# Performance work log

Measured on AMD Instinct MI355X. Metric: run time of the kernel, lower is better.

The kernel has to match this reference:

```python
import jax, jax.numpy as jnp
import numpy as np

N = 8192
IN_C = 512
OUT_C = 512


def setup_inputs() -> dict:
    key = jax.random.key(0)
    k1, k2, k3 = jax.random.split(key, 3)
    x = jax.random.normal(k1, (N, IN_C), dtype=jnp.float32)
    adj = jax.random.uniform(k2, (N, N), dtype=jnp.float32)
    # torch.rand initializer for the weight (uniform [0,1))
    w = jax.random.uniform(k3, (IN_C, OUT_C), dtype=jnp.float32)
    return {"x": x, "adj": adj, "w": w}


def reference(x, adj, w):
    # A = adj + I
    A = adj + jnp.eye(adj.shape[0], dtype=adj.dtype)
    # D_hat = diag(deg)^{-1/2}; diagonal inverse + sqrt == elementwise rsqrt of degrees
    deg = jnp.sum(A, axis=1)                      # [N]
    d_inv_sqrt = jax.lax.rsqrt(deg)               # [N]
    # A_hat = D_hat @ A @ D_hat == row/col scaling (same math, no dense inverse)
    A_hat = A * d_inv_sqrt[:, None] * d_inv_sqrt[None, :]
    mm_1 = A_hat @ x                              # [N, in_c]
    return jax.nn.elu(mm_1 @ w)                   # [N, out_c]
```

## Files before the change

### kernel.cpp

```cpp
#include <hip/hip_runtime.h>

#define NN 8192
#define CC 512

typedef __attribute__((ext_vector_type(8))) short short8;
typedef __attribute__((ext_vector_type(4))) float f32x4;
typedef unsigned short ushort_t;

__device__ __forceinline__ unsigned short f2bf(float f) {
    unsigned int u = __float_as_uint(f);
    u += 0x7FFF + ((u >> 16) & 1);
    return (unsigned short)(u >> 16);
}

__device__ __forceinline__ void gload_lds16(const void* g, void* l) {
    __builtin_amdgcn_global_load_lds((const __attribute__((address_space(1))) unsigned int*)g,
                                     (__attribute__((address_space(3))) unsigned int*)l,
                                     16, 0, 0);
}

__global__ __launch_bounds__(256) void k_rowsum_cvt(const float* __restrict__ adj,
                                                    float* __restrict__ ds,
                                                    ushort_t* __restrict__ adj16) {
    int row = blockIdx.x;
    const float4* p = (const float4*)(adj + (size_t)row * NN);
    ushort4* q = (ushort4*)(adj16 + (size_t)row * NN);
    float s = 0.f;
#pragma unroll
    for (int i = 0; i < 8; ++i) {
        float4 v = p[threadIdx.x + i * 256];
        s += (v.x + v.y) + (v.z + v.w);
        ushort4 u;
        u.x = f2bf(v.x); u.y = f2bf(v.y); u.z = f2bf(v.z); u.w = f2bf(v.w);
        q[threadIdx.x + i * 256] = u;
    }
#pragma unroll
    for (int off = 32; off > 0; off >>= 1) s += __shfl_down(s, off, 64);
    __shared__ float partial[4];
    if ((threadIdx.x & 63) == 0) partial[threadIdx.x >> 6] = s;
    __syncthreads();
    if (threadIdx.x == 0) {
        float deg = ((partial[0] + partial[1]) + (partial[2] + partial[3])) + 1.0f;
        ds[row] = rsqrtf(deg);
    }
}

__global__ __launch_bounds__(256) void k_rowsum(const float* __restrict__ adj,
                                                float* __restrict__ ds) {
    int row = blockIdx.x;
    const float4* p = (const float4*)(adj + (size_t)row * NN);
    float s = 0.f;
#pragma unroll
    for (int i = 0; i < 8; ++i) {
        float4 v = p[threadIdx.x + i * 256];
        s += (v.x + v.y) + (v.z + v.w);
    }
#pragma unroll
    for (int off = 32; off > 0; off >>= 1) s += __shfl_down(s, off, 64);
    __shared__ float partial[4];
    if ((threadIdx.x & 63) == 0) partial[threadIdx.x >> 6] = s;
    __syncthreads();
    if (threadIdx.x == 0) {
        float deg = ((partial[0] + partial[1]) + (partial[2] + partial[3])) + 1.0f;
        ds[row] = rsqrtf(deg);
    }
}

__global__ __launch_bounds__(256) void k_transpose(const float* __restrict__ in,
                                                   ushort_t* __restrict__ out,
                                                   const float* __restrict__ scale,
                                                   int R, int C) {
    __shared__ float tile[64][65];
    int r0 = blockIdx.x * 64, c0 = blockIdx.y * 64;
    int t = threadIdx.x;
    int cl = t & 63;
    int rl0 = t >> 6;
#pragma unroll
    for (int i = 0; i < 16; ++i) {
        int r = rl0 + i * 4;
        float v = in[(size_t)(r0 + r) * C + c0 + cl];
        float sc = scale ? scale[r0 + r] : 1.0f;
        tile[r][cl] = v * sc;
    }
    __syncthreads();
#pragma unroll
    for (int i = 0; i < 16; ++i) {
        int c = rl0 + i * 4;
        int r = cl;
        out[(size_t)(c0 + c) * R + r0 + r] = f2bf(tile[r][c]);
    }
}

__global__ __launch_bounds__(512, 2) void k_gemm1c(const ushort_t* __restrict__ adj16,
                                                   const ushort_t* __restrict__ yt,
                                                   float* __restrict__ part) {
    __shared__ __align__(16) ushort_t As[4][256 * 32];
    __shared__ __align__(16) ushort_t Bs[4][256 * 32];

    int t = threadIdx.x;
    int wid = t >> 6, lane = t & 63;

    int gid = blockIdx.x;
    int xcd = gid & 7, slot = gid >> 3;
    int cb = slot & 1;
    int u = (slot >> 1) + 16 * xcd;
    int rb = u & 31, ks = u >> 5;
    int rowBase = rb * 256, colBase = cb * 256;
    int kt0 = ks * 64;

    int wr = wid >> 2, wc = wid & 3;
    int fr = lane & 15, fq = lane >> 4;

    int row0 = t >> 2, c0 = t & 3;
    int sw0 = (c0 ^ ((row0 >> 1) & 3)) << 3;
    const ushort_t* aSrc0 = adj16 + (size_t)(rowBase + row0) * NN + sw0;
    const ushort_t* aSrc1 = adj16 + (size_t)(rowBase + row0 + 128) * NN + sw0;
    const ushort_t* bSrc0 = yt + (size_t)(colBase + row0) * NN + sw0;
    const ushort_t* bSrc1 = yt + (size_t)(colBase + row0 + 128) * NN + sw0;

    auto stage = [&](int buf, int kt) {
        int ko = kt * 32;
        gload_lds16(aSrc0 + ko, (char*)As[buf] + wid * 1024);
        gload_lds16(aSrc1 + ko, (char*)As[buf] + 8192 + wid * 1024);
        gload_lds16(bSrc0 + ko, (char*)Bs[buf] + wid * 1024);
        gload_lds16(bSrc1 + ko, (char*)Bs[buf] + 8192 + wid * 1024);
    };

    f32x4 acc[8][4] = {};
    int sws = (fq ^ ((fr >> 1) & 3)) << 4;

    stage(0, kt0 + 0);
    stage(1, kt0 + 1);
    stage(2, kt0 + 2);

    for (int j = 0; j < 64; ++j) {
        stage((j + 3) & 3, kt0 + ((j + 3) & 63));
        asm volatile("s_waitcnt vmcnt(12)" ::: "memory");
        __builtin_amdgcn_sched_barrier(0);
        __builtin_amdgcn_s_barrier();
        __builtin_amdgcn_sched_barrier(0);

        const char* Ab = (const char*)As[j & 3];
        const char* Bb = (const char*)Bs[j & 3];
        short8 af[8], bfr[4];
#pragma unroll
        for (int m = 0; m < 8; ++m)
            af[m] = *(const short8*)(Ab + (wr * 128 + m * 16 + fr) * 64 + sws);
#pragma unroll
        for (int n = 0; n < 4; ++n)
            bfr[n] = *(const short8*)(Bb + (wc * 64 + n * 16 + fr) * 64 + sws);

        __builtin_amdgcn_s_setprio(1);
#pragma unroll
        for (int m = 0; m < 8; ++m)
#pragma unroll
            for (int n = 0; n < 4; ++n)
                acc[m][n] = __builtin_amdgcn_mfma_f32_16x16x32_bf16(af[m], bfr[n], acc[m][n], 0, 0, 0);
        __builtin_amdgcn_s_setprio(0);
        __builtin_amdgcn_sched_barrier(0);
        __builtin_amdgcn_s_barrier();
        __builtin_amdgcn_sched_barrier(0);
    }

#pragma unroll
    for (int m = 0; m < 8; ++m) {
#pragma unroll
        for (int j = 0; j < 4; ++j) {
            int gr = rowBase + wr * 128 + m * 16 + fq * 4 + j;
            float* dst = &part[((size_t)ks * NN + gr) * CC];
#pragma unroll
            for (int n = 0; n < 4; ++n) {
                int gc = colBase + wc * 64 + n * 16 + fr;
                dst[gc] = acc[m][n][j];
            }
        }
    }
}

template <int MODE>
__global__ __launch_bounds__(256, 4) void k_gemm1(const float* __restrict__ adj,
                                                  const ushort_t* __restrict__ yt,
                                                  const float* __restrict__ ds,
                                                  const float* __restrict__ x,
                                                  ushort_t* __restrict__ mm1,
                                                  float* __restrict__ part) {
    __shared__ __align__(16) ushort_t As[128 * 64];
    __shared__ __align__(16) ushort_t Bs[128 * 64];

    int t = threadIdx.x;
    int wid = t >> 6, lane = t & 63;

    int rowBase, colBase, kt0, ktN, ks;
    if (MODE == 0) {
        int bid = blockIdx.x;
        bid = (bid & 7) * 32 + (bid >> 3);
        colBase = (bid & 3) * 128;
        rowBase = (bid >> 2) * 128;
        kt0 = 0; ktN = NN / 64; ks = 0;
    } else {
        int gid = blockIdx.x;
        int xcd = gid & 7, slot = gid >> 3;
        int cb = slot & 3;
        int g = (slot >> 2) * 8 + xcd;
        int rb = g & 63; ks = g >> 6;
        rowBase = rb * 128; colBase = cb * 128;
        kt0 = ks * (NN / 64 / 4); ktN = kt0 + NN / 64 / 4;
    }

    int ar = t >> 4;
    int ac4 = t & 15;
    const float* aptr = adj + (size_t)(rowBase + ar) * NN + ac4 * 4;
    int brow0 = t >> 3;
    int bs = t & 7;

    float4 areg[8];

    auto loadA = [&](int kt) {
        const float* p = aptr + kt * 64;
#pragma unroll
        for (int i = 0; i < 8; ++i)
            areg[i] = *(const float4*)(p + (size_t)i * 16 * NN);
    };
    auto writeA = [&]() {
#pragma unroll
        for (int i = 0; i < 8; ++i) {
            int row = i * 16 + ar;
            ushort4 u;
            u.x = f2bf(areg[i].x); u.y = f2bf(areg[i].y);
            u.z = f2bf(areg[i].z); u.w = f2bf(areg[i].w);
            *(ushort4*)((char*)As + row * 128 + ((ac4 * 8) ^ ((row & 7) << 4))) = u;
        }
    };
    auto stageB = [&](int kt) {
#pragma unroll
        for (int j = 0; j < 4; ++j) {
            int row = j * 32 + brow0;
            gload_lds16((const char*)(yt + (size_t)(colBase + row) * NN + kt * 64 +
                                      ((bs ^ (row & 7)) << 3)),
                        (char*)Bs + j * 4096 + wid * 1024);
        }
    };

    f32x4 acc[4][4] = {};
    int wr = wid >> 1, wc = wid & 1;
    int fr = lane & 15, fq = lane >> 4;

    loadA(kt0);
    for (int kt = kt0; kt < ktN; ++kt) {
        writeA();
        stageB(kt);
        __syncthreads();
        if (kt + 1 < ktN) loadA(kt + 1);
#pragma unroll
        for (int ks2 = 0; ks2 < 2; ++ks2) {
            short8 af[4], bf[4];
#pragma unroll
            for (int m = 0; m < 4; ++m) {
                int row = wr * 64 + m * 16 + fr;
                af[m] = *(const short8*)((const char*)As + row * 128 +
                                         ((ks2 * 64 + fq * 16) ^ ((row & 7) << 4)));
            }
#pragma unroll
            for (int n = 0; n < 4; ++n) {
                int col = wc * 64 + n * 16 + fr;
                bf[n] = *(const short8*)((const char*)Bs + col * 128 +
                                         ((ks2 * 64 + fq * 16) ^ ((col & 7) << 4)));
            }
#pragma unroll
            for (int m = 0; m < 4; ++m)
#pragma unroll
                for (int n = 0; n < 4; ++n)
                    acc[m][n] = __builtin_amdgcn_mfma_f32_16x16x32_bf16(af[m], bf[n], acc[m][n], 0, 0, 0);
        }
        __syncthreads();
    }

#pragma unroll
    for (int m = 0; m < 4; ++m) {
#pragma unroll
        for (int j = 0; j < 4; ++j) {
            int gr = rowBase + wr * 64 + m * 16 + fq * 4 + j;
            float dsr = (MODE == 0) ? ds[gr] : 0.f;
#pragma unroll
            for (int n = 0; n < 4; ++n) {
                int gc = colBase + wc * 64 + n * 16 + fr;
                float p = acc[m][n][j];
                if (MODE == 0) {
                    float v = dsr * (p + dsr * x[(size_t)gr * CC + gc]);
                    mm1[(size_t)gr * CC + gc] = f2bf(v);
                } else {
                    part[((size_t)ks * NN + gr) * CC + gc] = p;
                }
            }
        }
    }
}

__global__ __launch_bounds__(256) void k_finish(const float* __restrict__ part,
                                                const float* __restrict__ ds,
                                                const float* __restrict__ x,
                                                ushort_t* __restrict__ mm1,
                                                int nsplit) {
    size_t i = (size_t)blockIdx.x * 256 + threadIdx.x;
    const f32x4* p = (const f32x4*)part;
    const size_t stride = (size_t)NN * CC / 4;
    f32x4 s = p[i];
    for (int k = 1; k < nsplit; ++k) s += p[i + (size_t)k * stride];
    int row = (int)(i >> 7);
    float d = ds[row];
    f32x4 xv = ((const f32x4*)x)[i];
    ushort4 u;
    u.x = f2bf(d * (s[0] + d * xv[0]));
    u.y = f2bf(d * (s[1] + d * xv[1]));
    u.z = f2bf(d * (s[2] + d * xv[2]));
    u.w = f2bf(d * (s[3] + d * xv[3]));
    ((ushort4*)mm1)[i] = u;
}

__global__ __launch_bounds__(256, 2) void k_gemm2(const ushort_t* __restrict__ mm1,
                                                  const ushort_t* __restrict__ wt,
                                                  float* __restrict__ out) {
    __shared__ __align__(16) ushort_t As[128 * 64];
    __shared__ __align__(16) ushort_t Bs[128 * 64];

    int t = threadIdx.x;
    int wid = t >> 6, lane = t & 63;
    int bid = blockIdx.x;
    bid = (bid & 7) * 32 + (bid >> 3);
    int cb = bid & 3, rb = bid >> 2;
    int rowBase = rb * 128, colBase = cb * 128;

    int srow0 = t >> 3, ss = t & 7;

    f32x4 acc[4][4] = {};
    int wr = wid >> 1, wc = wid & 1;
    int fr = lane & 15, fq = lane >> 4;

    for (int kt = 0; kt < CC / 64; ++kt) {
#pragma unroll
        for (int j = 0; j < 4; ++j) {
            int row = j * 32 + srow0;
            gload_lds16((const char*)(mm1 + (size_t)(rowBase + row) * CC + kt * 64 +
                                      ((ss ^ (row & 7)) << 3)),
                        (char*)As + j * 4096 + wid * 1024);
            gload_lds16((const char*)(wt + (size_t)(colBase + row) * CC + kt * 64 +
                                      ((ss ^ (row & 7)) << 3)),
                        (char*)Bs + j * 4096 + wid * 1024);
        }
        __syncthreads();
#pragma unroll
        for (int ks = 0; ks < 2; ++ks) {
            short8 af[4], bf[4];
#pragma unroll
            for (int m = 0; m < 4; ++m) {
                int row = wr * 64 + m * 16 + fr;
                af[m] = *(const short8*)((const char*)As + row * 128 +
                                         ((ks * 64 + fq * 16) ^ ((row & 7) << 4)));
            }
#pragma unroll
            for (int n = 0; n < 4; ++n) {
                int col = wc * 64 + n * 16 + fr;
                bf[n] = *(const short8*)((const char*)Bs + col * 128 +
                                         ((ks * 64 + fq * 16) ^ ((col & 7) << 4)));
            }
#pragma unroll
            for (int m = 0; m < 4; ++m)
#pragma unroll
                for (int n = 0; n < 4; ++n)
                    acc[m][n] = __builtin_amdgcn_mfma_f32_16x16x32_bf16(af[m], bf[n], acc[m][n], 0, 0, 0);
        }
        __syncthreads();
    }

#pragma unroll
    for (int m = 0; m < 4; ++m) {
#pragma unroll
        for (int j = 0; j < 4; ++j) {
            int gr = rowBase + wr * 64 + m * 16 + fq * 4 + j;
#pragma unroll
            for (int n = 0; n < 4; ++n) {
                int gc = colBase + wc * 64 + n * 16 + fr;
                float v = acc[m][n][j];
                out[(size_t)gr * CC + gc] = v > 0.f ? v : expm1f(v);
            }
        }
    }
}

extern "C" void kernel_launch(void* const* d_in, const int* in_sizes, int n_in,
                              void* d_out, int out_size, void* d_ws, size_t ws_size,
                              hipStream_t stream) {
    const float* x   = (const float*)d_in[0];
    const float* adj = (const float*)d_in[1];
    const float* w   = (const float*)d_in[2];
    float* out = (float*)d_out;

    char* ws = (char*)d_ws;
    size_t off = 0;
    float*    ds  = (float*)(ws + off);  off += 32u << 10;
    ushort_t* yt  = (ushort_t*)(ws + off);  off += 8u << 20;
    ushort_t* wt  = (ushort_t*)(ws + off);  off += 512u << 10;
    ushort_t* mm1 = (ushort_t*)(ws + off);  off += 8u << 20;
    float*    part = (float*)(ws + off);
    const size_t partBytes = 4 * (size_t)NN * CC * 4;
    ushort_t* adj16 = (ushort_t*)(ws + off + partBytes);
    const size_t adjBytes = (size_t)NN * NN * 2;

    if (ws_size >= off + partBytes + adjBytes) {
        k_rowsum_cvt<<<NN, 256, 0, stream>>>(adj, ds, adj16);
        k_transpose<<<dim3(NN / 64, CC / 64), 256, 0, stream>>>(x, yt, ds, NN, CC);
        k_transpose<<<dim3(CC / 64, CC / 64), 256, 0, stream>>>(w, wt, nullptr, CC, CC);
        k_gemm1c<<<256, 512, 0, stream>>>(adj16, yt, part);
        k_finish<<<NN * CC / 4 / 256, 256, 0, stream>>>(part, ds, x, mm1, 4);
    } else if (ws_size >= off + partBytes) {
        k_rowsum<<<NN, 256, 0, stream>>>(adj, ds);
        k_transpose<<<dim3(NN / 64, CC / 64), 256, 0, stream>>>(x, yt, ds, NN, CC);
        k_transpose<<<dim3(CC / 64, CC / 64), 256, 0, stream>>>(w, wt, nullptr, CC, CC);
        k_gemm1<1><<<1024, 256, 0, stream>>>(adj, yt, ds, x, mm1, part);
        k_finish<<<NN * CC / 4 / 256, 256, 0, stream>>>(part, ds, x, mm1, 4);
    } else {
        k_rowsum<<<NN, 256, 0, stream>>>(adj, ds);
        k_transpose<<<dim3(NN / 64, CC / 64), 256, 0, stream>>>(x, yt, ds, NN, CC);
        k_transpose<<<dim3(CC / 64, CC / 64), 256, 0, stream>>>(w, wt, nullptr, CC, CC);
        k_gemm1<0><<<256, 256, 0, stream>>>(adj, yt, ds, x, mm1, part);
    }

    k_gemm2<<<256, 256, 0, stream>>>(mm1, wt, out);
}
```

Before: 228.5 us.

## Reassociate to compute x@W first, store bf16 split-K partials, restage gemm1

The computation is reordered as A_hat @ (x @ W). The small x@W GEMM runs first, its result is scaled and transposed, and the large adjacency GEMM then feeds a finish kernel that applies the degree scaling, adds the identity term and applies ELU. This removes the separate second GEMM over the mm1 intermediate. Split-K partials are now stored as bf16 instead of fp32, which halves partial-sum traffic but adds rounding error. The large GEMM's LDS pipeline changes from 4-stage to double-buffered, with global loads interleaved between half-tile MFMA groups.

```diff
diff --git a/kernel.cpp b/kernel.cpp
--- a/kernel.cpp
+++ b/kernel.cpp
@@ -11,6 +11,9 @@
     unsigned int u = __float_as_uint(f);
     u += 0x7FFF + ((u >> 16) & 1);
     return (unsigned short)(u >> 16);
+}
+__device__ __forceinline__ float bf2f(unsigned short u) {
+    return __uint_as_float(((unsigned int)u) << 16);
 }
 
 __device__ __forceinline__ void gload_lds16(const void* g, void* l) {
@@ -64,6 +67,15 @@
         float deg = ((partial[0] + partial[1]) + (partial[2] + partial[3])) + 1.0f;
         ds[row] = rsqrtf(deg);
     }
+}
+
+__global__ __launch_bounds__(256) void k_cvt(const float* __restrict__ in,
+                                             ushort_t* __restrict__ out) {
+    size_t i = (size_t)blockIdx.x * 256 + threadIdx.x;
+    float4 v = ((const float4*)in)[i];
+    ushort4 u;
+    u.x = f2bf(v.x); u.y = f2bf(v.y); u.z = f2bf(v.z); u.w = f2bf(v.w);
+    ((ushort4*)out)[i] = u;
 }
 
 __global__ __launch_bounds__(256) void k_transpose(const float* __restrict__ in,
@@ -91,14 +103,86 @@
     }
 }
 
-__global__ __launch_bounds__(512, 2) void k_gemm1c(const ushort_t* __restrict__ adj16,
-                                                   const ushort_t* __restrict__ yt,
-                                                   float* __restrict__ part) {
-    __shared__ __align__(16) ushort_t As[4][256 * 32];
-    __shared__ __align__(16) ushort_t Bs[4][256 * 32];
+template <bool ELU>
+__global__ __launch_bounds__(256, 2) void k_gemm2t(const ushort_t* __restrict__ A,
+                                                   const ushort_t* __restrict__ Bt,
+                                                   float* __restrict__ out) {
+    __shared__ __align__(16) ushort_t As[128 * 64];
+    __shared__ __align__(16) ushort_t Bs[128 * 64];
 
     int t = threadIdx.x;
     int wid = t >> 6, lane = t & 63;
+    int bid = blockIdx.x;
+    bid = (bid & 7) * 32 + (bid >> 3);
+    int cb = bid & 3, rb = bid >> 2;
+    int rowBase = rb * 128, colBase = cb * 128;
+
+    int srow0 = t >> 3, ss = t & 7;
+
+    f32x4 acc[4][4] = {};
+    int wr = wid >> 1, wc = wid & 1;
+    int fr = lane & 15, fq = lane >> 4;
+
+    for (int kt = 0; kt < CC / 64; ++kt) {
+#pragma unroll
+        for (int j = 0; j < 4; ++j) {
+            int row = j * 32 + srow0;
+            gload_lds16((const char*)(A + (size_t)(rowBase + row) * CC + kt * 64 +
+                                      ((ss ^ (row & 7)) << 3)),
+                        (char*)As + j * 4096 + wid * 1024);
+            gload_lds16((const char*)(Bt + (size_t)(colBase + row) * CC + kt * 64 +
+                                      ((ss ^ (row & 7)) << 3)),
+                        (char*)Bs + j * 4096 + wid * 1024);
+        }
+        __syncthreads();
+#pragma unroll
+        for (int ks = 0; ks < 2; ++ks) {
+            short8 af[4], bf[4];
+#pragma unroll
+            for (int m = 0; m < 4; ++m) {
+                int row = wr * 64 + m * 16 + fr;
+                af[m] = *(const short8*)((const char*)As + row * 128 +
+                                         ((ks * 64 + fq * 16) ^ ((row & 7) << 4)));
+            }
+#pragma unroll
+            for (int n = 0; n < 4; ++n) {
+                int col = wc * 64 + n * 16 + fr;
+                bf[n] = *(const short8*)((const char*)Bs + col * 128 +
+                                         ((ks * 64 + fq * 16) ^ ((col & 7) << 4)));
+            }
+#pragma unroll
+            for (int m = 0; m < 4; ++m)
+#pragma unroll
+                for (int n = 0; n < 4; ++n)
+                    acc[m][n] = __builtin_amdgcn_mfma_f32_16x16x32_bf16(af[m], bf[n], acc[m][n], 0, 0, 0);
+        }
+        __syncthreads();
+    }
+
+#pragma unroll
+    for (int m = 0; m < 4; ++m) {
+#pragma unroll
+        for (int j = 0; j < 4; ++j) {
+            int gr = rowBase + wr * 64 + m * 16 + fq * 4 + j;
+#pragma unroll
+            for (int n = 0; n < 4; ++n) {
+                int gc = colBase + wc * 64 + n * 16 + fr;
+                float v = acc[m][n][j];
+                out[(size_t)gr * CC + gc] = ELU ? (v > 0.f ? v : expm1f(v)) : v;
+            }
+        }
+    }
+}
+
+__global__ __launch_bounds__(512, 2) void k_gemm1d(const ushort_t* __restrict__ adj16,
+                                                   const ushort_t* __restrict__ yt2,
+                                                   ushort_t* __restrict__ part16) {
+    __shared__ __align__(16) ushort_t Al[2][2][2][128 * 32];
+    __shared__ __align__(16) ushort_t Bl[2][2][2][128 * 32];
+
+    int t = threadIdx.x;
+    int wid = t >> 6, lane = t & 63;
+    int fr = lane & 15, fq = lane >> 4;
 
     int gid = blockIdx.x;
     int xcd = gid & 7, slot = gid >> 3;
@@ -106,113 +190,142 @@
     int u = (slot >> 1) + 16 * xcd;
     int rb = u & 31, ks = u >> 5;
     int rowBase = rb * 256, colBase = cb * 256;
-    int kt0 = ks * 64;
+    size_t kt0 = (size_t)ks * 2048;
 
     int wr = wid >> 2, wc = wid & 3;
-    int fr = lane & 15, fq = lane >> 4;
-
-    int row0 = t >> 2, c0 = t & 3;
-    int sw0 = (c0 ^ ((row0 >> 1) & 3)) << 3;
-    const ushort_t* aSrc0 = adj16 + (size_t)(rowBase + row0) * NN + sw0;
-    const ushort_t* aSrc1 = adj16 + (size_t)(rowBase + row0 + 128) * NN + sw0;
-    const ushort_t* bSrc0 = yt + (size_t)(colBase + row0) * NN + sw0;
-    const ushort_t* bSrc1 = yt + (size_t)(colBase + row0 + 128) * NN + sw0;
-
-    auto stage = [&](int buf, int kt) {
-        int ko = kt * 32;
-        gload_lds16(aSrc0 + ko, (char*)As[buf] + wid * 1024);
-        gload_lds16(aSrc1 + ko, (char*)As[buf] + 8192 + wid * 1024);
-        gload_lds16(bSrc0 + ko, (char*)Bs[buf] + wid * 1024);
-        gload_lds16(bSrc1 + ko, (char*)Bs[buf] + 8192 + wid * 1024);
-    };
+
+    int srow = t >> 2;
+    int sw = ((t & 3) ^ ((srow >> 1) & 3)) << 3;
+    const ushort_t* aBase = adj16 + (size_t)(rowBase + srow) * NN + sw;
+    const ushort_t* bBase = yt2 + (size_t)(colBase + srow) * NN + sw;
 
     f32x4 acc[8][4] = {};
     int sws = (fq ^ ((fr >> 1) & 3)) << 4;
 
-    stage(0, kt0 + 0);
-    stage(1, kt0 + 1);
-    stage(2, kt0 + 2);
-
-    for (int j = 0; j < 64; ++j) {
-        stage((j + 3) & 3, kt0 + ((j + 3) & 63));
-        asm volatile("s_waitcnt vmcnt(12)" ::: "memory");
-        __builtin_amdgcn_sched_barrier(0);
-        __builtin_amdgcn_s_barrier();
-        __builtin_amdgcn_sched_barrier(0);
-
-        const char* Ab = (const char*)As[j & 3];
-        const char* Bb = (const char*)Bs[j & 3];
-        short8 af[8], bfr[4];
-#pragma unroll
-        for (int m = 0; m < 8; ++m)
-            af[m] = *(const short8*)(Ab + (wr * 128 + m * 16 + fr) * 64 + sws);
-#pragma unroll
-        for (int n = 0; n < 4; ++n)
-            bfr[n] = *(const short8*)(Bb + (wc * 64 + n * 16 + fr) * 64 + sws);
-
-        __builtin_amdgcn_s_setprio(1);
-#pragma unroll
-        for (int m = 0; m < 8; ++m)
+#pragma unroll
+    for (int tt = 0; tt < 2; ++tt)
+#pragma unroll
+        for (int h = 0; h < 2; ++h) {
+            gload_lds16(aBase + (size_t)(h * 128) * NN + kt0 + tt * 32,
+                        (char*)Al[0][tt][h] + wid * 1024);
+            gload_lds16(bBase + (size_t)(h * 128) * NN + kt0 + tt * 32,
+                        (char*)Bl[0][tt][h] + wid * 1024);
+        }
+    asm volatile("s_waitcnt vmcnt(0)" ::: "memory");
+    __syncthreads();
+
+    for (int i = 0; i < 32; ++i) {
+        int cur = i & 1, nxt = cur ^ 1;
+        size_t Kn = kt0 + (size_t)(((i + 1) & 31) * 64);
+#pragma unroll
+        for (int tt = 0; tt < 2; ++tt) {
+            const char* Ab = (const char*)Al[cur][tt][wr];
+            const char* Bb = (const char*)Bl[cur][tt][wc >> 1];
+            int bcol0 = (wc & 1) * 64;
+            short8 af0[4], bf[4];
+#pragma unroll
+            for (int m = 0; m < 4; ++m)
+                af0[m] = *(const short8*)(Ab + (m * 16 + fr) * 64 + sws);
 #pragma unroll
             for (int n = 0; n < 4; ++n)
-                acc[m][n] = __builtin_amdgcn_mfma_f32_16x16x32_bf16(af[m], bfr[n], acc[m][n], 0, 0, 0);
-        __builtin_amdgcn_s_setprio(0);
-        __builtin_amdgcn_sched_barrier(0);
-        __builtin_amdgcn_s_barrier();
-        __builtin_amdgcn_sched_barrier(0);
+                bf[n] = *(const short8*)(Bb + (bcol0 + n * 16 + fr) * 64 + sws);
+            gload_lds16(aBase + Kn + tt * 32, (char*)Al[nxt][tt][0] + wid * 1024);
+            gload_lds16(aBase + (size_t)128 * NN + Kn + tt * 32, (char*)Al[nxt][tt][1] + wid * 1024);
+            asm volatile("s_waitcnt vmcnt(4)" ::: "memory");
+            __builtin_amdgcn_sched_barrier(0);
+            __builtin_amdgcn_s_barrier();
+            __builtin_amdgcn_sched_barrier(0);
+            __builtin_amdgcn_s_setprio(1);
+#pragma unroll
+            for (int m = 0; m < 4; ++m)
+#pragma unroll
+                for (int n = 0; n < 4; ++n)
+                    acc[m][n] = __builtin_amdgcn_mfma_f32_16x16x32_bf16(af0[m], bf[n], acc[m][n], 0, 0, 0);
+            __builtin_amdgcn_s_setprio(0);
+            __builtin_amdgcn_sched_barrier(0);
+            __builtin_amdgcn_s_barrier();
+            __builtin_amdgcn_sched_barrier(0);
+            short8 af1[4];
+#pragma unroll
+            for (int m = 0; m < 4; ++m)
+                af1[m] = *(const short8*)(Ab + ((64 + m * 16 + fr) * 64) + sws);
+            gload_lds16(bBase + Kn + tt * 32, (char*)Bl[nxt][tt][0] + wid * 1024);
+            gload_lds16(bBase + (size_t)128 * NN + Kn + tt * 32, (char*)Bl[nxt][tt][1] + wid * 1024);
+            asm volatile("s_waitcnt vmcnt(4)" ::: "memory");
+            __builtin_amdgcn_sched_barrier(0);
+            __builtin_amdgcn_s_barrier();
+            __builtin_amdgcn_sched_barrier(0);
+            __builtin_amdgcn_s_setprio(1);
+#pragma unroll
+            for (int m = 0; m < 4; ++m)
+#pragma unroll
+                for (int n = 0; n < 4; ++n)
+                    acc[4 + m][n] = __builtin_amdgcn_mfma_f32_16x16x32_bf16(af1[m], bf[n], acc[4 + m][n], 0, 0, 0);
+            __builtin_amdgcn_s_setprio(0);
+            __builtin_amdgcn_sched_barrier(0);
+            __builtin_amdgcn_s_barrier();
+            __builtin_amdgcn_sched_barrier(0);
+        }
     }
 
 #pragma unroll
     for (int m = 0; m < 8; ++m) {
 #pragma unroll
-        for (int j = 0; j < 4; ++j) {
-            int gr = rowBase + wr * 128 + m * 16 + fq * 4 + j;
-            float* dst = &part[((size_t)ks * NN + gr) * CC];
-#pragma unroll
-            for (int n = 0; n < 4; ++n) {
-                int gc = colBase + wc * 64 + n * 16 + fr;
-                dst[gc] = acc[m][n][j];
-            }
-        }
-    }
-}
-
-template <int MODE>
-__global__ __launch_bounds__(256, 4) void k_gemm1(const float* __restrict__ adj,
-                                                  const ushort_t* __restrict__ yt,
-                                                  const float* __restrict__ ds,
-                                                  const float* __restrict__ x,
-                                                  ushort_t* __restrict__ mm1,
-                                                  float* __restrict__ part) {
+        for (int jj = 0; jj < 4; ++jj) {
+            int gr = rowBase + wr * 128 + m * 16 + fq * 4 + jj;
+            ushort_t* dst = part16 + ((size_t)ks * NN + gr) * CC + colBase;
+#pragma unroll
+            for (int n = 0; n < 4; ++n)
+                dst[wc * 64 + n * 16 + fr] = f2bf(acc[m][n][jj]);
+        }
+    }
+}
+
+__global__ __launch_bounds__(256) void k_finish2(const ushort_t* __restrict__ part16,
+                                                 const float* __restrict__ ds,
+                                                 const float* __restrict__ z,
+                                                 float* __restrict__ out) {
+    size_t i = (size_t)blockIdx.x * 256 + threadIdx.x;
+    const size_t stride = (size_t)NN * CC / 4;
+    float s0 = 0.f, s1 = 0.f, s2 = 0.f, s3 = 0.f;
+#pragma unroll
+    for (int k = 0; k < 4; ++k) {
+        ushort4 p = ((const ushort4*)part16)[i + k * stride];
+        s0 += bf2f(p.x); s1 += bf2f(p.y); s2 += bf2f(p.z); s3 += bf2f(p.w);
+    }
+    int row = (int)(i >> 7);
+    float d = ds[row];
+    float d2 = d * d;
+    f32x4 zv = ((const f32x4*)z)[i];
+    f32x4 o;
+    float v;
+    v = d * s0 + d2 * zv[0]; o[0] = v > 0.f ? v : expm1f(v);
+    v = d * s1 + d2 * zv[1]; o[1] = v > 0.f ? v : expm1f(v);
+    v = d * s2 + d2 * zv[2]; o[2] = v > 0.f ? v : expm1f(v);
+    v = d * s3 + d2 * zv[3]; o[3] = v > 0.f ? v : expm1f(v);
+    ((f32x4*)out)[i] = o;
+}
+
+__global__ __launch_bounds__(256, 4) void k_gemm1_fb(const float* __restrict__ adj,
+                                                     const ushort_t* __restrict__ yt,
+                                                     const float* __restrict__ ds,
+                                                     const float* __restrict__ x,
+                                                     ushort_t* __restrict__ mm1) {
     __shared__ __align__(16) ushort_t As[128 * 64];
     __shared__ __align__(16) ushort_t Bs[128 * 64];
 
     int t = threadIdx.x;
     int wid = t >> 6, lane = t & 63;
-
-    int rowBase, colBase, kt0, ktN, ks;
-    if (MODE == 0) {
-        int bid = blockIdx.x;
-        bid = (bid & 7) * 32 + (bid >> 3);
-        colBase = (bid & 3) * 128;
-        rowBase = (bid >> 2) * 128;
-        kt0 = 0; ktN = NN / 64; ks = 0;
-    } else {
-        int gid = blockIdx.x;
-        int xcd = gid & 7, slot = gid >> 3;
-        int cb = slot & 3;
-        int g = (slot >> 2) * 8 + xcd;
-        int rb = g & 63; ks = g >> 6;
-        rowBase = rb * 128; colBase = cb * 128;
-        kt0 = ks * (NN / 64 / 4); ktN = kt0 + NN / 64 / 4;
-    }
+    int bid = blockIdx.x;
+    bid = (bid & 7) * 32 + (bid >> 3);
+    int colBase = (bid & 3) * 128;
+    int rowBase = (bid >> 2) * 128;
 
     int ar = t >> 4;
     int ac4 = t & 15;
     const float* aptr = adj + (size_t)(rowBase + ar) * NN + ac4 * 4;
     int brow0 = t >> 3;
     int bs = t & 7;
-
     float4 areg[8];
 
     auto loadA = [&](int kt) {
@@ -231,7 +344,14 @@
             *(ushort4*)((char*)As + row * 128 + ((ac4 * 8) ^ ((row & 7) << 4))) = u;
         }
     };
-    auto stageB = [&](int kt) {
+
+    f32x4 acc[4][4] = {};
+    int wr = wid >> 1, wc = wid & 1;
+    int fr = lane & 15, fq = lane >> 4;
+
+    loadA(0);
+    for (int kt = 0; kt < NN / 64; ++kt) {
+        writeA();
 #pragma unroll
         for (int j = 0; j < 4; ++j) {
             int row = j * 32 + brow0;
@@ -239,18 +359,8 @@
                                       ((bs ^ (row & 7)) << 3)),
                         (char*)Bs + j * 4096 + wid * 1024);
         }
-    };
-
-    f32x4 acc[4][4] = {};
-    int wr = wid >> 1, wc = wid & 1;
-    int fr = lane & 15, fq = lane >> 4;
-
-    loadA(kt0);
-    for (int kt = kt0; kt < ktN; ++kt) {
-        writeA();
-        stageB(kt);
         __syncthreads();
-        if (kt + 1 < ktN) loadA(kt + 1);
+        if (kt + 1 < NN / 64) loadA(kt + 1);
 #pragma unroll
         for (int ks2 = 0; ks2 < 2; ++ks2) {
             short8 af[4], bf[4];
@@ -280,108 +390,12 @@
 #pragma unroll
         for (int j = 0; j < 4; ++j) {
             int gr = rowBase + wr * 64 + m * 16 + fq * 4 + j;
-            float dsr = (MODE == 0) ? ds[gr] : 0.f;
+            float dsr = ds[gr];
 #pragma unroll
             for (int n = 0; n < 4; ++n) {
                 int gc = colBase + wc * 64 + n * 16 + fr;
-                float p = acc[m][n][j];
-                if (MODE == 0) {
-                    float v = dsr * (p + dsr * x[(size_t)gr * CC + gc]);
-                    mm1[(size_t)gr * CC + gc] = f2bf(v);
-                } else {
-                    part[((size_t)ks * NN + gr) * CC + gc] = p;
-                }
-            }
-        }
-    }
-}
-
-__global__ __launch_bounds__(256) void k_finish(const float* __restrict__ part,
-                                                const float* __restrict__ ds,
-                                                const float* __restrict__ x,
-                                                ushort_t* __restrict__ mm1,
-                                                int nsplit) {
-    size_t i = (size_t)blockIdx.x * 256 + threadIdx.x;
-    const f32x4* p = (const f32x4*)part;
-    const size_t stride = (size_t)NN * CC / 4;
-    f32x4 s = p[i];
-    for (int k = 1; k < nsplit; ++k) s += p[i + (size_t)k * stride];
-    int row = (int)(i >> 7);
-    float d = ds[row];
-    f32x4 xv = ((const f32x4*)x)[i];
-    ushort4 u;
-    u.x = f2bf(d * (s[0] + d * xv[0]));
-    u.y = f2bf(d * (s[1] + d * xv[1]));
-    u.z = f2bf(d * (s[2] + d * xv[2]));
-    u.w = f2bf(d * (s[3] + d * xv[3]));
-    ((ushort4*)mm1)[i] = u;
-}
-
-__global__ __launch_bounds__(256, 2) void k_gemm2(const ushort_t* __restrict__ mm1,
-                                                  const ushort_t* __restrict__ wt,
-                                                  float* __restrict__ out) {
-    __shared__ __align__(16) ushort_t As[128 * 64];
-    __shared__ __align__(16) ushort_t Bs[128 * 64];
-
-    int t = threadIdx.x;
-    int wid = t >> 6, lane = t & 63;
-    int bid = blockIdx.x;
-    bid = (bid & 7) * 32 + (bid >> 3);
-    int cb = bid & 3, rb = bid >> 2;
-    int rowBase = rb * 128, colBase = cb * 128;
-
-    int srow0 = t >> 3, ss = t & 7;
-
-    f32x4 acc[4][4] = {};
-    int wr = wid >> 1, wc = wid & 1;
-    int fr = lane & 15, fq = lane >> 4;
-
-    for (int kt = 0; kt < CC / 64; ++kt) {
-#pragma unroll
-        for (int j = 0; j < 4; ++j) {
-            int row = j * 32 + srow0;
-            gload_lds16((const char*)(mm1 + (size_t)(rowBase + row) * CC + kt * 64 +
-                                      ((ss ^ (row & 7)) << 3)),
-                        (char*)As + j * 4096 + wid * 1024);
-            gload_lds16((const char*)(wt + (size_t)(colBase + row) * CC + kt * 64 +
-                                      ((ss ^ (row & 7)) << 3)),
-                        (char*)Bs + j * 4096 + wid * 1024);
-        }
-        __syncthreads();
-#pragma unroll
-        for (int ks = 0; ks < 2; ++ks) {
-            short8 af[4], bf[4];
-#pragma unroll
-            for (int m = 0; m < 4; ++m) {
-                int row = wr * 64 + m * 16 + fr;
-                af[m] = *(const short8*)((const char*)As + row * 128 +
-                                         ((ks * 64 + fq * 16) ^ ((row & 7) << 4)));
-            }
-#pragma unroll
-            for (int n = 0; n < 4; ++n) {
-                int col = wc * 64 + n * 16 + fr;
-                bf[n] = *(const short8*)((const char*)Bs + col * 128 +
-                                         ((ks * 64 + fq * 16) ^ ((col & 7) << 4)));
-            }
-#pragma unroll
-            for (int m = 0; m < 4; ++m)
-#pragma unroll
-                for (int n = 0; n < 4; ++n)
-                    acc[m][n] = __builtin_amdgcn_mfma_f32_16x16x32_bf16(af[m], bf[n], acc[m][n], 0, 0, 0);
-        }
-        __syncthreads();
-    }
-
-#pragma unroll
-    for (int m = 0; m < 4; ++m) {
-#pragma unroll
-        for (int j = 0; j < 4; ++j) {
-            int gr = rowBase + wr * 64 + m * 16 + fq * 4 + j;
-#pragma unroll
-            for (int n = 0; n < 4; ++n) {
-                int gc = colBase + wc * 64 + n * 16 + fr;
-                float v = acc[m][n][j];
-                out[(size_t)gr * CC + gc] = v > 0.f ? v : expm1f(v);
+                float v = dsr * (acc[m][n][j] + dsr * x[(size_t)gr * CC + gc]);
+                mm1[(size_t)gr * CC + gc] = f2bf(v);
             }
         }
     }
@@ -400,30 +414,26 @@
     float*    ds  = (float*)(ws + off);  off += 32u << 10;
     ushort_t* yt  = (ushort_t*)(ws + off);  off += 8u << 20;
     ushort_t* wt  = (ushort_t*)(ws + off);  off += 512u << 10;
-    ushort_t* mm1 = (ushort_t*)(ws + off);  off += 8u << 20;
-    float*    part = (float*)(ws + off);
-    const size_t partBytes = 4 * (size_t)NN * CC * 4;
-    ushort_t* adj16 = (ushort_t*)(ws + off + partBytes);
+    ushort_t* xb  = (ushort_t*)(ws + off);  off += 8u << 20;
+    float*    z   = (float*)(ws + off);  off += 16u << 20;
+    ushort_t* part16 = (ushort_t*)(ws + off);  off += 32u << 20;
+    ushort_t* adj16  = (ushort_t*)(ws + off);
     const size_t adjBytes = (size_t)NN * NN * 2;
 
-    if (ws_size >= off + partBytes + adjBytes) {
+    if (ws_size >= off + adjBytes) {
         k_rowsum_cvt<<<NN, 256, 0, stream>>>(adj, ds, adj16);
-        k_transpose<<<dim3(NN / 64, CC / 64), 256, 0, stream>>>(x, yt, ds, NN, CC);
+        k_cvt<<<NN * CC / 4 / 256, 256, 0, stream>>>(x, xb);
         k_transpose<<<dim3(CC / 64, CC / 64), 256, 0, stream>>>(w, wt, nullptr, CC, CC);
-        k_gemm1c<<<256, 512, 0, stream>>>(adj16, yt, part);
-        k_finish<<<NN * CC / 4 / 256, 256, 0, stream>>>(part, ds, x, mm1, 4);
-    } else if (ws_size >= off + partBytes) {
+        k_gemm2t<false><<<256, 256, 0, stream>>>(xb, wt, z);
+        k_transpose<<<dim3(NN / 64, CC / 64), 256, 0, stream>>>(z, yt, ds, NN, CC);
+        k_gemm1d<<<256, 512, 0, stream>>>(adj16, yt, part16);
+        k_finish2<<<NN * CC / 4 / 256, 256, 0, stream>>>(part16, ds, z, out);
+    } else {
+        ushort_t* mm1 = xb;
         k_rowsum<<<NN, 256, 0, stream>>>(adj, ds);
         k_transpose<<<dim3(NN / 64, CC / 64), 256, 0, stream>>>(x, yt, ds, NN, CC);
         k_transpose<<<dim3(CC / 64, CC / 64), 256, 0, stream>>>(w, wt, nullptr, CC, CC);
-        k_gemm1<1><<<1024, 256, 0, stream>>>(adj, yt, ds, x, mm1, part);
-        k_finish<<<NN * CC / 4 / 256, 256, 0, stream>>>(part, ds, x, mm1, 4);
-    } else {
-        k_rowsum<<<NN, 256, 0, stream>>>(adj, ds);
-        k_transpose<<<dim3(NN / 64, CC / 64), 256, 0, stream>>>(x, yt, ds, NN, CC);
-        k_transpose<<<dim3(CC / 64, CC / 64), 256, 0, stream>>>(w, wt, nullptr, CC, CC);
-        k_gemm1<0><<<256, 256, 0, stream>>>(adj, yt, ds, x, mm1, part);
-    }
-
-    k_gemm2<<<256, 256, 0, stream>>>(mm1, wt, out);
-}
+        k_gemm1_fb<<<256, 256, 0, stream>>>(adj, yt, ds, x, mm1);
+        k_gemm2t<true><<<256, 256, 0, stream>>>(mm1, wt, out);
+    }
+}
```

Result: faster. 214.7 us (-6.0%).
